# Optimization experiments

Measured on AMD Instinct MI355X. Metric: run time of the kernel, lower is better.

The kernel has to match this reference:

```python
import jax, jax.numpy as jnp
import numpy as np

N_NODES = 10000
N_EDGES = 70000
H = 128
L = 15  # message_passing_num
NODE_IN = 11  # 2 frame dims + 9 one-hot node types
EDGE_IN = 3
LN_EPS = 1e-5


def _mlp(x, W1, b1, W2, b2):
    return jax.nn.relu(x @ W1 + b1) @ W2 + b2


def _mlp_ln(x, W1, b1, W2, b2, g, b):
    h = _mlp(x, W1, b1, W2, b2)
    mu = jnp.mean(h, axis=-1, keepdims=True)
    var = jnp.var(h, axis=-1, keepdims=True)
    return (h - mu) * jax.lax.rsqrt(var + LN_EPS) * g + b


def setup_inputs() -> dict:
    key = jax.random.key(0)
    ks = iter(jax.random.split(key, 40))
    rn = lambda shp, s: (jax.random.normal(next(ks), shp, jnp.float32) * s)
    inp = {
        "node_type": jax.random.randint(next(ks), (N_NODES,), 0, 9, jnp.int32),
        "edge_index": jax.random.randint(next(ks), (2, N_EDGES), 0, N_NODES, jnp.int32),
        "frames": jax.random.normal(next(ks), (N_NODES, 2), jnp.float32),
        "edge_feats": jax.random.normal(next(ks), (N_EDGES, EDGE_IN), jnp.float32),
        "node_norm_mean": jax.random.normal(next(ks), (NODE_IN,), jnp.float32) * 0.1,
        "node_norm_std": jax.random.uniform(next(ks), (NODE_IN,), jnp.float32) + 0.5,
        "out_norm_mean": jax.random.normal(next(ks), (2,), jnp.float32) * 0.1,
        "out_norm_std": jax.random.uniform(next(ks), (2,), jnp.float32) + 0.5,
        # encoder node MLP (11 -> 128 -> 128, LayerNorm)
        "enc_nW1": rn((NODE_IN, H), NODE_IN ** -0.5), "enc_nb1": jnp.zeros((H,)),
        "enc_nW2": rn((H, H), H ** -0.5), "enc_nb2": jnp.zeros((H,)),
        "enc_nlng": jnp.ones((H,)), "enc_nlnb": jnp.zeros((H,)),
        # encoder edge MLP (3 -> 128 -> 128, LayerNorm)
        "enc_eW1": rn((EDGE_IN, H), EDGE_IN ** -0.5), "enc_eb1": jnp.zeros((H,)),
        "enc_eW2": rn((H, H), H ** -0.5), "enc_eb2": jnp.zeros((H,)),
        "enc_elng": jnp.ones((H,)), "enc_elnb": jnp.zeros((H,)),
        # L GNN blocks, stacked. Edge MLP: 3H -> H -> H (+LN); Node MLP: 2H -> H -> H (+LN)
        "eb_W1": rn((L, 3 * H, H), (3 * H) ** -0.5), "eb_b1": jnp.zeros((L, H)),
        "eb_W2": rn((L, H, H), H ** -0.5), "eb_b2": jnp.zeros((L, H)),
        "eb_lng": jnp.ones((L, H)), "eb_lnb": jnp.zeros((L, H)),
        "nb_W1": rn((L, 2 * H, H), (2 * H) ** -0.5), "nb_b1": jnp.zeros((L, H)),
        "nb_W2": rn((L, H, H), H ** -0.5), "nb_b2": jnp.zeros((L, H)),
        "nb_lng": jnp.ones((L, H)), "nb_lnb": jnp.zeros((L, H)),
        # decoder MLP (128 -> 128 -> 2, no LayerNorm)
        "dec_W1": rn((H, H), H ** -0.5), "dec_b1": jnp.zeros((H,)),
        "dec_W2": rn((H, 2), H ** -0.5), "dec_b2": jnp.zeros((2,)),
    }
    return inp


def reference(node_type, edge_index, frames, edge_feats,
              node_norm_mean, node_norm_std, out_norm_mean, out_norm_std,
              enc_nW1, enc_nb1, enc_nW2, enc_nb2, enc_nlng, enc_nlnb,
              enc_eW1, enc_eb1, enc_eW2, enc_eb2, enc_elng, enc_elnb,
              eb_W1, eb_b1, eb_W2, eb_b2, eb_lng, eb_lnb,
              nb_W1, nb_b1, nb_W2, nb_b2, nb_lng, nb_lnb,
              dec_W1, dec_b1, dec_W2, dec_b2):
    n_nodes = frames.shape[0]
    senders, receivers = edge_index[0], edge_index[1]

    # update_node_attr: concat(frames, one_hot(type, 9)) then normalize (eval mode)
    one_hot = jax.nn.one_hot(node_type, 9, dtype=frames.dtype)
    node_feats = jnp.concatenate([frames, one_hot], axis=1)  # [N, 11]
    node_attr = (node_feats - node_norm_mean) / node_norm_std

    # Encoder
    x = _mlp_ln(node_attr, enc_nW1, enc_nb1, enc_nW2, enc_nb2, enc_nlng, enc_nlnb)   # [N, H]
    e = _mlp_ln(edge_feats, enc_eW1, enc_eb1, enc_eW2, enc_eb2, enc_elng, enc_elnb)  # [E, H]

    # Processor: L residual GNN blocks (EdgeBlock then NodeBlock)
    def block(carry, p):
        x, e = carry
        (eW1, eb1, eW2, eb2, eg, ebn, nW1, nb1, nW2, nb2, ng, nbn) = p
        e_in = jnp.concatenate([x[senders], x[receivers], e], axis=-1)  # [E, 3H]
        e_new = _mlp_ln(e_in, eW1, eb1, eW2, eb2, eg, ebn)              # [E, H]
        agg = jax.ops.segment_sum(e_new, receivers, num_segments=n_nodes)  # [N, H]
        x_new = _mlp_ln(jnp.concatenate([x, agg], axis=-1), nW1, nb1, nW2, nb2, ng, nbn)
        return (x + x_new, e + e_new), None

    (x, e), _ = jax.lax.scan(
        block, (x, e),
        (eb_W1, eb_b1, eb_W2, eb_b2, eb_lng, eb_lnb,
         nb_W1, nb_b1, nb_W2, nb_b2, nb_lng, nb_lnb))

    # Decoder (no LayerNorm) + inverse output normalization (eval path)
    decoded = _mlp(x, dec_W1, dec_b1, dec_W2, dec_b2)  # [N, 2]
    velocity_update = decoded * out_norm_std + out_norm_mean
    return frames + velocity_update
```

## Files before the change

### kernel.cpp

```cpp
#include <hip/hip_runtime.h>
#include <hip/hip_bf16.h>

#define N_NODES 10000
#define N_EDGES 70000
#define NPAD 10112
#define EPAD 70016
#define H 128
#define NLAYERS 15
constexpr float LN_EPS = 1e-5f;

typedef __attribute__((ext_vector_type(8))) short short8;
typedef __attribute__((ext_vector_type(4))) float f32x4;

__device__ __forceinline__ float bf2f(unsigned int ulo16) {
    return __uint_as_float(ulo16 << 16);
}
__device__ __forceinline__ unsigned short f2bf(float f) {
    unsigned int x = __float_as_uint(f);
    x += 0x7fffu + ((x >> 16) & 1u);
    return (unsigned short)(x >> 16);
}

__global__ void prep_node(const int* __restrict__ nt, const float* __restrict__ frames,
                          const float* __restrict__ nm, const float* __restrict__ ns,
                          unsigned short* __restrict__ a16b) {
    int i = blockIdx.x * blockDim.x + threadIdx.x;
    if (i >= NPAD * 32) return;
    int n = i >> 5, k = i & 31;
    float v = 0.f;
    if (n < N_NODES && k < 11) {
        float raw = (k < 2) ? frames[n * 2 + k] : ((nt[n] == (k - 2)) ? 1.f : 0.f);
        v = (raw - nm[k]) / ns[k];
    }
    a16b[i] = f2bf(v);
}

__global__ void prep_edge(const float* __restrict__ ef, unsigned short* __restrict__ a4b) {
    int i = blockIdx.x * blockDim.x + threadIdx.x;
    if (i >= EPAD * 32) return;
    int e = i >> 5, k = i & 31;
    float v = (e < N_EDGES && k < 3) ? ef[e * 3 + k] : 0.f;
    a4b[i] = f2bf(v);
}

__global__ void transpose_w_tiled(const float* __restrict__ w, unsigned short* __restrict__ wt,
                                  int Kr, int Kp, int nmat) {
    __shared__ float T[32][33];
    int nkt = Kp / 32;
    int bid = blockIdx.x;
    int m = bid / (nkt * 4);
    int rest = bid % (nkt * 4);
    int kt = rest / 4, ct = rest % 4;
    int t = threadIdx.x;
    int tc = t & 31, tr = t >> 5;
#pragma unroll
    for (int rr = 0; rr < 4; ++rr) {
        int k = kt * 32 + tr + rr * 8;
        int c = ct * 32 + tc;
        T[tr + rr * 8][tc] = (k < Kr) ? w[((size_t)m * Kr + k) * H + c] : 0.f;
    }
    __syncthreads();
#pragma unroll
    for (int rr = 0; rr < 4; ++rr) {
        int c = ct * 32 + tr + rr * 8;
        int k = kt * 32 + tc;
        wt[((size_t)m * H + c) * Kp + k] = f2bf(T[tc][tr + rr * 8]);
    }
}

__global__ void hist_kernel(const int* __restrict__ rcv, int* __restrict__ counts) {
    int j = blockIdx.x * blockDim.x + threadIdx.x;
    if (j < N_EDGES) atomicAdd(&counts[rcv[j]], 1);
}

__global__ void scan_kernel(const int* __restrict__ counts, int* __restrict__ starts) {
    __shared__ int part[1024];
    const int CH = 10;
    int t = threadIdx.x;
    int base = t * CH;
    int loc[CH];
    int s = 0;
#pragma unroll
    for (int i = 0; i < CH; i++) {
        int idx = base + i;
        int c = (idx < N_NODES) ? counts[idx] : 0;
        loc[i] = s;
        s += c;
    }
    part[t] = s;
    __syncthreads();
    for (int off = 1; off < 1024; off <<= 1) {
        int v = (t >= off) ? part[t - off] : 0;
        __syncthreads();
        part[t] += v;
        __syncthreads();
    }
    int pre = (t > 0) ? part[t - 1] : 0;
#pragma unroll
    for (int i = 0; i < CH; i++) {
        int idx = base + i;
        if (idx < N_NODES) starts[idx] = pre + loc[i];
    }
}

__global__ void scatter_kernel(const int* __restrict__ rcv, const int* __restrict__ starts,
                               int* __restrict__ cursor, int* __restrict__ esorted) {
    int j = blockIdx.x * blockDim.x + threadIdx.x;
    if (j >= N_EDGES) return;
    int r = rcv[j];
    int p = starts[r] + atomicAdd(&cursor[r], 1);
    esorted[p] = j;
}

__global__ void agg_kernel(const unsigned short* __restrict__ enew,
                           const int* __restrict__ esorted,
                           const int* __restrict__ starts,
                           const int* __restrict__ counts,
                           unsigned short* __restrict__ aggb) {
    int n = blockIdx.x * 8 + (threadIdx.x >> 5);
    int l = threadIdx.x & 31;
    if (n >= N_NODES) return;
    float a0 = 0.f, a1 = 0.f, a2 = 0.f, a3 = 0.f;
    int s0 = starts[n], cnt = counts[n];
    for (int j = 0; j < cnt; ++j) {
        int e = esorted[s0 + j];
        uint2 v = *reinterpret_cast<const uint2*>(enew + (size_t)e * H + l * 4);
        a0 += bf2f(v.x & 0xffffu);
        a1 += bf2f(v.x >> 16);
        a2 += bf2f(v.y & 0xffffu);
        a3 += bf2f(v.y >> 16);
    }
    uint2 o;
    o.x = (unsigned int)f2bf(a0) | ((unsigned int)f2bf(a1) << 16);
    o.y = (unsigned int)f2bf(a2) | ((unsigned int)f2bf(a3) << 16);
    *reinterpret_cast<uint2*>(aggb + (size_t)n * H + l * 4) = o;
}

template <int K1, int AMODE, int EPI, int WR>
__launch_bounds__(256)
__global__ void mlp_fused(const unsigned short* __restrict__ A,
                          const unsigned short* __restrict__ Xb,
                          const unsigned short* __restrict__ Eb,
                          const unsigned short* __restrict__ Gb,
                          const int* __restrict__ snd,
                          const int* __restrict__ rcv,
                          const unsigned short* __restrict__ Bt1,
                          const float* __restrict__ bias1,
                          const unsigned short* __restrict__ Bt2,
                          const float* __restrict__ bias2,
                          const float* __restrict__ lng,
                          const float* __restrict__ lnb,
                          unsigned short* __restrict__ out_bf,
                          float* __restrict__ out_fp,
                          unsigned short* __restrict__ enew_bf,
                          int nrows) {
    constexpr int BK1 = (K1 >= 64) ? 64 : K1;
    constexpr int SA = BK1 + 8;
    constexpr int SB = 72;
    constexpr int SH = H + 8;
    constexpr int BM = 64 * WR;
    __shared__ __attribute__((aligned(16))) unsigned short As[BM * SA];
    __shared__ __attribute__((aligned(16))) unsigned short Bs[H * SB];
    __shared__ __attribute__((aligned(16))) unsigned short Hs[BM * SH];

    const int tid = threadIdx.x;
    const int wave = tid >> 6;
    const int lane = tid & 63;
    const int l15 = lane & 15;
    const int lhi = lane >> 4;
    const int row0 = blockIdx.x * BM;
    const int wrow = wave * 16 * WR;

    f32x4 acc[WR][8];
#pragma unroll
    for (int i = 0; i < WR; i++)
#pragma unroll
        for (int j = 0; j < 8; j++) acc[i][j] = (f32x4){0.f, 0.f, 0.f, 0.f};

    for (int kc = 0; kc < K1; kc += BK1) {
        constexpr int KQ = BK1 / 8;
        constexpr int LPT_A = BM * KQ / 256;
#pragma unroll
        for (int it = 0; it < LPT_A; ++it) {
            int q = tid + it * 256;
            int r = q / KQ;
            int kq = q % KQ;
            int gk = kc + kq * 8;
            int grow = row0 + r;
            const unsigned short* src;
            if (AMODE == 0) {
                src = A + (size_t)grow * K1 + gk;
            } else if (AMODE == 1) {
                int e = (grow < nrows) ? grow : 0;
                if (gk < H)          src = Xb + (size_t)snd[e] * H + gk;
                else if (gk < 2 * H) src = Xb + (size_t)rcv[e] * H + (gk - H);
                else                 src = Eb + (size_t)grow * H + (gk - 2 * H);
            } else {
                if (gk < H) src = Xb + (size_t)grow * H + gk;
                else        src = Gb + (size_t)grow * H + (gk - H);
            }
            uint4 v = *reinterpret_cast<const uint4*>(src);
            *reinterpret_cast<uint4*>(&As[r * SA + kq * 8]) = v;
        }
        constexpr int LPT_B = H * KQ / 256;
#pragma unroll
        for (int it = 0; it < LPT_B; ++it) {
            int q = tid + it * 256;
            int c = q / KQ;
            int kq = q % KQ;
            uint4 v = *reinterpret_cast<const uint4*>(Bt1 + (size_t)c * K1 + kc + kq * 8);
            *reinterpret_cast<uint4*>(&Bs[c * SB + kq * 8]) = v;
        }
        __syncthreads();
#pragma unroll
        for (int ks = 0; ks < BK1 / 32; ++ks) {
            short8 af[WR];
#pragma unroll
            for (int i = 0; i < WR; ++i)
                af[i] = *reinterpret_cast<const short8*>(
                    &As[(wrow + i * 16 + l15) * SA + ks * 32 + lhi * 8]);
#pragma unroll
            for (int j = 0; j < 8; ++j) {
                short8 bfr = *reinterpret_cast<const short8*>(
                    &Bs[(j * 16 + l15) * SB + ks * 32 + lhi * 8]);
#pragma unroll
                for (int i = 0; i < WR; ++i)
                    acc[i][j] = __builtin_amdgcn_mfma_f32_16x16x32_bf16(af[i], bfr, acc[i][j], 0, 0, 0);
            }
        }
        __syncthreads();
    }

    {
        float b1v[8];
#pragma unroll
        for (int j = 0; j < 8; ++j) b1v[j] = bias1[j * 16 + l15];
#pragma unroll
        for (int i = 0; i < WR; ++i)
#pragma unroll
            for (int r = 0; r < 4; ++r) {
                int rl = wrow + i * 16 + lhi * 4 + r;
#pragma unroll
                for (int j = 0; j < 8; ++j) {
                    float v = acc[i][j][r] + b1v[j];
                    Hs[rl * SH + j * 16 + l15] = f2bf(v > 0.f ? v : 0.f);
                }
            }
    }

#pragma unroll
    for (int i = 0; i < WR; i++)
#pragma unroll
        for (int j = 0; j < 8; j++) acc[i][j] = (f32x4){0.f, 0.f, 0.f, 0.f};

    for (int kc = 0; kc < H; kc += 64) {
        __syncthreads();
#pragma unroll
        for (int it = 0; it < 4; ++it) {
            int q = tid + it * 256;
            int c = q >> 3;
            int kq = q & 7;
            uint4 v = *reinterpret_cast<const uint4*>(Bt2 + (size_t)c * H + kc + kq * 8);
            *reinterpret_cast<uint4*>(&Bs[c * SB + kq * 8]) = v;
        }
        __syncthreads();
#pragma unroll
        for (int ks = 0; ks < 2; ++ks) {
            short8 af[WR];
#pragma unroll
            for (int i = 0; i < WR; ++i)
                af[i] = *reinterpret_cast<const short8*>(
                    &Hs[(wrow + i * 16 + l15) * SH + kc + ks * 32 + lhi * 8]);
#pragma unroll
            for (int j = 0; j < 8; ++j) {
                short8 bfr = *reinterpret_cast<const short8*>(
                    &Bs[(j * 16 + l15) * SB + ks * 32 + lhi * 8]);
#pragma unroll
                for (int i = 0; i < WR; ++i)
                    acc[i][j] = __builtin_amdgcn_mfma_f32_16x16x32_bf16(af[i], bfr, acc[i][j], 0, 0, 0);
            }
        }
    }

    float bv[8], gv[8], lv[8];
#pragma unroll
    for (int j = 0; j < 8; ++j) {
        bv[j] = bias2[j * 16 + l15];
        gv[j] = lng[j * 16 + l15];
        lv[j] = lnb[j * 16 + l15];
    }

#pragma unroll
    for (int i = 0; i < WR; ++i) {
#pragma unroll
        for (int r = 0; r < 4; ++r) {
            int row = row0 + wrow + i * 16 + lhi * 4 + r;
            float v[8];
            float s = 0.f, s2 = 0.f;
#pragma unroll
            for (int j = 0; j < 8; ++j) {
                v[j] = acc[i][j][r] + bv[j];
                s += v[j];
                s2 += v[j] * v[j];
            }
#pragma unroll
            for (int m = 1; m < 16; m <<= 1) {
                s += __shfl_xor(s, m);
                s2 += __shfl_xor(s2, m);
            }
            float mean = s * (1.f / 128.f);
            float var = s2 * (1.f / 128.f) - mean * mean;
            float rstd = rsqrtf(var + LN_EPS);
            if (row < nrows) {
#pragma unroll
                for (int j = 0; j < 8; ++j) {
                    float o = (v[j] - mean) * rstd * gv[j] + lv[j];
                    size_t off = (size_t)row * H + j * 16 + l15;
                    if (EPI == 1) {
                        out_fp[off] = o;
                        out_bf[off] = f2bf(o);
                    } else if (EPI == 2) {
                        float nx = out_fp[off] + o;
                        out_fp[off] = nx;
                        out_bf[off] = f2bf(nx);
                    } else {
                        float ne = out_fp[off] + o;
                        out_fp[off] = ne;
                        out_bf[off] = f2bf(ne);
                        enew_bf[off] = f2bf(o);
                    }
                }
            }
        }
    }
}

__global__ void decoder_kernel(const float* __restrict__ x,
                               const float* __restrict__ frames,
                               const float* __restrict__ W1, const float* __restrict__ b1,
                               const float* __restrict__ W2, const float* __restrict__ b2,
                               const float* __restrict__ omean, const float* __restrict__ ostd,
                               float* __restrict__ outp) {
    __shared__ float xr[H];
    __shared__ float hr[H];
    __shared__ float red[2][2];
    int n = blockIdx.x;
    int t = threadIdx.x;
    xr[t] = x[n * H + t];
    __syncthreads();
    float acc = 0.f;
#pragma unroll 8
    for (int k = 0; k < H; k++) acc += xr[k] * W1[k * H + t];
    hr[t] = fmaxf(acc + b1[t], 0.f);
    __syncthreads();
    float p0 = hr[t] * W2[t * 2 + 0];
    float p1 = hr[t] * W2[t * 2 + 1];
#pragma unroll
    for (int m = 1; m < 64; m <<= 1) {
        p0 += __shfl_xor(p0, m);
        p1 += __shfl_xor(p1, m);
    }
    if ((t & 63) == 0) { red[t >> 6][0] = p0; red[t >> 6][1] = p1; }
    __syncthreads();
    if (t < 2) {
        float d = red[0][t] + red[1][t] + b2[t];
        outp[n * 2 + t] = frames[n * 2 + t] + d * ostd[t] + omean[t];
    }
}

extern "C" void kernel_launch(void* const* d_in, const int* in_sizes, int n_in,
                              void* d_out, int out_size, void* d_ws, size_t ws_size,
                              hipStream_t stream) {
    (void)in_sizes; (void)n_in; (void)out_size; (void)ws_size;
    const int*   node_type  = (const int*)  d_in[0];
    const int*   edge_index = (const int*)  d_in[1];
    const float* frames     = (const float*)d_in[2];
    const float* edge_feats = (const float*)d_in[3];
    const float* nmean      = (const float*)d_in[4];
    const float* nstd       = (const float*)d_in[5];
    const float* omean      = (const float*)d_in[6];
    const float* ostd       = (const float*)d_in[7];
    const float* enc_nW1    = (const float*)d_in[8];
    const float* enc_nb1    = (const float*)d_in[9];
    const float* enc_nW2    = (const float*)d_in[10];
    const float* enc_nb2    = (const float*)d_in[11];
    const float* enc_nlng   = (const float*)d_in[12];
    const float* enc_nlnb   = (const float*)d_in[13];
    const float* enc_eW1    = (const float*)d_in[14];
    const float* enc_eb1    = (const float*)d_in[15];
    const float* enc_eW2    = (const float*)d_in[16];
    const float* enc_eb2    = (const float*)d_in[17];
    const float* enc_elng   = (const float*)d_in[18];
    const float* enc_elnb   = (const float*)d_in[19];
    const float* eb_W1      = (const float*)d_in[20];
    const float* eb_b1      = (const float*)d_in[21];
    const float* eb_W2      = (const float*)d_in[22];
    const float* eb_b2      = (const float*)d_in[23];
    const float* eb_g       = (const float*)d_in[24];
    const float* eb_bn      = (const float*)d_in[25];
    const float* nb_W1      = (const float*)d_in[26];
    const float* nb_b1      = (const float*)d_in[27];
    const float* nb_W2      = (const float*)d_in[28];
    const float* nb_b2      = (const float*)d_in[29];
    const float* nb_g       = (const float*)d_in[30];
    const float* nb_bn      = (const float*)d_in[31];
    const float* dec_W1     = (const float*)d_in[32];
    const float* dec_b1     = (const float*)d_in[33];
    const float* dec_W2     = (const float*)d_in[34];
    const float* dec_b2     = (const float*)d_in[35];

    const int* snd = edge_index;
    const int* rcv = edge_index + N_EDGES;

    char* p = (char*)d_ws;
    auto alloc = [&](size_t bytes) {
        void* r = (void*)p;
        p += (bytes + 255) & ~(size_t)255;
        return r;
    };
    float* x_fp  = (float*)alloc((size_t)NPAD * H * 4);
    float* e_fp  = (float*)alloc((size_t)EPAD * H * 4);
    unsigned short* x_bf   = (unsigned short*)alloc((size_t)NPAD * H * 2);
    unsigned short* e_bf   = (unsigned short*)alloc((size_t)EPAD * H * 2);
    unsigned short* enew   = (unsigned short*)alloc((size_t)EPAD * H * 2);
    unsigned short* agg_bf = (unsigned short*)alloc((size_t)NPAD * H * 2);
    unsigned short* a16b   = (unsigned short*)alloc((size_t)NPAD * 32 * 2);
    unsigned short* a4b    = (unsigned short*)alloc((size_t)EPAD * 32 * 2);
    unsigned short* wt_en1 = (unsigned short*)alloc((size_t)128 * 32 * 2);
    unsigned short* wt_ee1 = (unsigned short*)alloc((size_t)128 * 32 * 2);
    unsigned short* wt_en2 = (unsigned short*)alloc((size_t)128 * 128 * 2);
    unsigned short* wt_ee2 = (unsigned short*)alloc((size_t)128 * 128 * 2);
    unsigned short* wt_eb1 = (unsigned short*)alloc((size_t)NLAYERS * 128 * 384 * 2);
    unsigned short* wt_eb2 = (unsigned short*)alloc((size_t)NLAYERS * 128 * 128 * 2);
    unsigned short* wt_nb1 = (unsigned short*)alloc((size_t)NLAYERS * 128 * 256 * 2);
    unsigned short* wt_nb2 = (unsigned short*)alloc((size_t)NLAYERS * 128 * 128 * 2);
    int* counts  = (int*)alloc((size_t)N_NODES * 4);
    int* starts  = (int*)alloc((size_t)N_NODES * 4);
    int* cursor  = (int*)alloc((size_t)N_NODES * 4);
    int* esorted = (int*)alloc((size_t)N_EDGES * 4);

    prep_node<<<(NPAD * 32 + 255) / 256, 256, 0, stream>>>(node_type, frames, nmean, nstd, a16b);
    prep_edge<<<(EPAD * 32 + 255) / 256, 256, 0, stream>>>(edge_feats, a4b);
    auto tw = [&](const float* w, unsigned short* wt, int Kr, int Kp, int nmat) {
        int blocks = nmat * (Kp / 32) * 4;
        transpose_w_tiled<<<blocks, 256, 0, stream>>>(w, wt, Kr, Kp, nmat);
    };
    tw(enc_nW1, wt_en1, 11, 32, 1);
    tw(enc_eW1, wt_ee1, 3, 32, 1);
    tw(enc_nW2, wt_en2, 128, 128, 1);
    tw(enc_eW2, wt_ee2, 128, 128, 1);
    tw(eb_W1, wt_eb1, 384, 384, NLAYERS);
    tw(eb_W2, wt_eb2, 128, 128, NLAYERS);
    tw(nb_W1, wt_nb1, 256, 256, NLAYERS);
    tw(nb_W2, wt_nb2, 128, 128, NLAYERS);

    hipMemsetAsync(counts, 0, (size_t)N_NODES * 4, stream);
    hipMemsetAsync(cursor, 0, (size_t)N_NODES * 4, stream);
    hist_kernel<<<(N_EDGES + 255) / 256, 256, 0, stream>>>(rcv, counts);
    scan_kernel<<<1, 1024, 0, stream>>>(counts, starts);
    scatter_kernel<<<(N_EDGES + 255) / 256, 256, 0, stream>>>(rcv, starts, cursor, esorted);

    const int gE = EPAD / 128;
    const int gN = NPAD / 64;
    const unsigned short* nu_ = nullptr;
    const int* ni_ = nullptr;
    unsigned short* nm_ = nullptr;

    mlp_fused<32, 0, 1, 1><<<gN, 256, 0, stream>>>(a16b, nu_, nu_, nu_, ni_, ni_,
        wt_en1, enc_nb1, wt_en2, enc_nb2, enc_nlng, enc_nlnb,
        x_bf, x_fp, nm_, N_NODES);
    mlp_fused<32, 0, 1, 2><<<gE, 256, 0, stream>>>(a4b, nu_, nu_, nu_, ni_, ni_,
        wt_ee1, enc_eb1, wt_ee2, enc_eb2, enc_elng, enc_elnb,
        e_bf, e_fp, nm_, N_EDGES);

    for (int l = 0; l < NLAYERS; ++l) {
        mlp_fused<384, 1, 3, 2><<<gE, 256, 0, stream>>>(nu_, x_bf, e_bf, nu_, snd, rcv,
            wt_eb1 + (size_t)l * 128 * 384, eb_b1 + l * H,
            wt_eb2 + (size_t)l * 128 * 128, eb_b2 + l * H, eb_g + l * H, eb_bn + l * H,
            e_bf, e_fp, enew, N_EDGES);
        agg_kernel<<<(N_NODES + 7) / 8, 256, 0, stream>>>(enew, esorted, starts, counts, agg_bf);
        mlp_fused<256, 2, 2, 1><<<gN, 256, 0, stream>>>(nu_, x_bf, nu_, agg_bf, ni_, ni_,
            wt_nb1 + (size_t)l * 128 * 256, nb_b1 + l * H,
            wt_nb2 + (size_t)l * 128 * 128, nb_b2 + l * H, nb_g + l * H, nb_bn + l * H,
            x_bf, x_fp, nm_, N_NODES);
    }

    decoder_kernel<<<N_NODES, 128, 0, stream>>>(x_fp, frames, dec_W1, dec_b1, dec_W2, dec_b2,
                                                omean, ostd, (float*)d_out);
}
```

Baseline: 1.181 ms.

## Pre-swizzle weights into MFMA fragment layout and drop LDS staging in MLP kernel

Measured after the change: 1.418 ms. +20.1%, slower.

```diff
diff --git a/kernel.cpp b/kernel.cpp
--- a/kernel.cpp
+++ b/kernel.cpp
@@ -43,8 +43,8 @@
     a4b[i] = f2bf(v);
 }
 
-__global__ void transpose_w_tiled(const float* __restrict__ w, unsigned short* __restrict__ wt,
-                                  int Kr, int Kp, int nmat) {
+__global__ void transpose_w_frag(const float* __restrict__ w, unsigned short* __restrict__ wt,
+                                 int Kr, int Kp, int nmat) {
     __shared__ float T[32][33];
     int nkt = Kp / 32;
     int bid = blockIdx.x;
@@ -64,7 +64,9 @@
     for (int rr = 0; rr < 4; ++rr) {
         int c = ct * 32 + tr + rr * 8;
         int k = kt * 32 + tc;
-        wt[((size_t)m * H + c) * Kp + k] = f2bf(T[tc][tr + rr * 8]);
+        size_t fidx = ((((size_t)m * nkt + (k >> 5)) * 8 + (c >> 4)) * 64
+                       + ((k >> 3) & 3) * 16 + (c & 15)) * 8 + (k & 7);
+        wt[fidx] = f2bf(T[tc][tr + rr * 8]);
     }
 }
 
@@ -117,118 +119,104 @@
                            const int* __restrict__ starts,
                            const int* __restrict__ counts,
                            unsigned short* __restrict__ aggb) {
-    int n = blockIdx.x * 8 + (threadIdx.x >> 5);
-    int l = threadIdx.x & 31;
+    int n = blockIdx.x * 16 + (threadIdx.x >> 4);
+    int l = threadIdx.x & 15;
     if (n >= N_NODES) return;
-    float a0 = 0.f, a1 = 0.f, a2 = 0.f, a3 = 0.f;
+    float a[8];
+#pragma unroll
+    for (int q = 0; q < 8; ++q) a[q] = 0.f;
     int s0 = starts[n], cnt = counts[n];
     for (int j = 0; j < cnt; ++j) {
         int e = esorted[s0 + j];
-        uint2 v = *reinterpret_cast<const uint2*>(enew + (size_t)e * H + l * 4);
-        a0 += bf2f(v.x & 0xffffu);
-        a1 += bf2f(v.x >> 16);
-        a2 += bf2f(v.y & 0xffffu);
-        a3 += bf2f(v.y >> 16);
-    }
-    uint2 o;
-    o.x = (unsigned int)f2bf(a0) | ((unsigned int)f2bf(a1) << 16);
-    o.y = (unsigned int)f2bf(a2) | ((unsigned int)f2bf(a3) << 16);
-    *reinterpret_cast<uint2*>(aggb + (size_t)n * H + l * 4) = o;
-}
-
-template <int K1, int AMODE, int EPI, int WR>
+        uint4 v = *reinterpret_cast<const uint4*>(enew + (size_t)e * H + l * 8);
+        a[0] += bf2f(v.x & 0xffffu); a[1] += bf2f(v.x >> 16);
+        a[2] += bf2f(v.y & 0xffffu); a[3] += bf2f(v.y >> 16);
+        a[4] += bf2f(v.z & 0xffffu); a[5] += bf2f(v.z >> 16);
+        a[6] += bf2f(v.w & 0xffffu); a[7] += bf2f(v.w >> 16);
+    }
+    uint4 o;
+    o.x = (unsigned int)f2bf(a[0]) | ((unsigned int)f2bf(a[1]) << 16);
+    o.y = (unsigned int)f2bf(a[2]) | ((unsigned int)f2bf(a[3]) << 16);
+    o.z = (unsigned int)f2bf(a[4]) | ((unsigned int)f2bf(a[5]) << 16);
+    o.w = (unsigned int)f2bf(a[6]) | ((unsigned int)f2bf(a[7]) << 16);
+    *reinterpret_cast<uint4*>(aggb + (size_t)n * H + l * 8) = o;
+}
+
+template <int K1, int AMODE, int EPI, int RW>
 __launch_bounds__(256)
-__global__ void mlp_fused(const unsigned short* __restrict__ A,
-                          const unsigned short* __restrict__ Xb,
-                          const unsigned short* __restrict__ Eb,
-                          const unsigned short* __restrict__ Gb,
-                          const int* __restrict__ snd,
-                          const int* __restrict__ rcv,
-                          const unsigned short* __restrict__ Bt1,
-                          const float* __restrict__ bias1,
-                          const unsigned short* __restrict__ Bt2,
-                          const float* __restrict__ bias2,
-                          const float* __restrict__ lng,
-                          const float* __restrict__ lnb,
-                          unsigned short* __restrict__ out_bf,
-                          float* __restrict__ out_fp,
-                          unsigned short* __restrict__ enew_bf,
-                          int nrows) {
-    constexpr int BK1 = (K1 >= 64) ? 64 : K1;
-    constexpr int SA = BK1 + 8;
-    constexpr int SB = 72;
+__global__ void mlp_wave(const unsigned short* __restrict__ A,
+                         const unsigned short* __restrict__ Xb,
+                         const unsigned short* __restrict__ Eb,
+                         const unsigned short* __restrict__ Gb,
+                         const int* __restrict__ snd,
+                         const int* __restrict__ rcv,
+                         const unsigned short* __restrict__ Bt1,
+                         const float* __restrict__ bias1,
+                         const unsigned short* __restrict__ Bt2,
+                         const float* __restrict__ bias2,
+                         const float* __restrict__ lng,
+                         const float* __restrict__ lnb,
+                         unsigned short* __restrict__ out_bf,
+                         float* __restrict__ out_fp,
+                         unsigned short* __restrict__ enew_bf,
+                         int nrows) {
     constexpr int SH = H + 8;
-    constexpr int BM = 64 * WR;
-    __shared__ __attribute__((aligned(16))) unsigned short As[BM * SA];
-    __shared__ __attribute__((aligned(16))) unsigned short Bs[H * SB];
-    __shared__ __attribute__((aligned(16))) unsigned short Hs[BM * SH];
+    __shared__ __attribute__((aligned(16))) unsigned short Hs[4 * 16 * RW * SH];
 
     const int tid = threadIdx.x;
     const int wave = tid >> 6;
     const int lane = tid & 63;
     const int l15 = lane & 15;
     const int lhi = lane >> 4;
-    const int row0 = blockIdx.x * BM;
-    const int wrow = wave * 16 * WR;
-
-    f32x4 acc[WR][8];
-#pragma unroll
-    for (int i = 0; i < WR; i++)
+    const int wrow0 = (blockIdx.x * 4 + wave) * (16 * RW);
+    unsigned short* Hw = Hs + wave * (16 * RW) * SH;
+
+    const unsigned short* pS[RW];
+    const unsigned short* pR[RW];
+    const unsigned short* pE[RW];
+#pragma unroll
+    for (int i = 0; i < RW; ++i) {
+        int grow = wrow0 + i * 16 + l15;
+        if (AMODE == 0) {
+            pS[i] = A + (size_t)grow * K1;
+        } else if (AMODE == 1) {
+            int e = (grow < nrows) ? grow : (nrows - 1);
+            pS[i] = Xb + (size_t)snd[e] * H;
+            pR[i] = Xb + (size_t)rcv[e] * H;
+            pE[i] = Eb + (size_t)grow * H;
+        } else {
+            pS[i] = Xb + (size_t)grow * H;
+            pR[i] = Gb + (size_t)grow * H;
+        }
+    }
+
+    f32x4 acc[RW][8];
+#pragma unroll
+    for (int i = 0; i < RW; i++)
 #pragma unroll
         for (int j = 0; j < 8; j++) acc[i][j] = (f32x4){0.f, 0.f, 0.f, 0.f};
 
-    for (int kc = 0; kc < K1; kc += BK1) {
-        constexpr int KQ = BK1 / 8;
-        constexpr int LPT_A = BM * KQ / 256;
-#pragma unroll
-        for (int it = 0; it < LPT_A; ++it) {
-            int q = tid + it * 256;
-            int r = q / KQ;
-            int kq = q % KQ;
-            int gk = kc + kq * 8;
-            int grow = row0 + r;
-            const unsigned short* src;
-            if (AMODE == 0) {
-                src = A + (size_t)grow * K1 + gk;
-            } else if (AMODE == 1) {
-                int e = (grow < nrows) ? grow : 0;
-                if (gk < H)          src = Xb + (size_t)snd[e] * H + gk;
-                else if (gk < 2 * H) src = Xb + (size_t)rcv[e] * H + (gk - H);
-                else                 src = Eb + (size_t)grow * H + (gk - 2 * H);
-            } else {
-                if (gk < H) src = Xb + (size_t)grow * H + gk;
-                else        src = Gb + (size_t)grow * H + (gk - H);
-            }
-            uint4 v = *reinterpret_cast<const uint4*>(src);
-            *reinterpret_cast<uint4*>(&As[r * SA + kq * 8]) = v;
+#pragma unroll 4
+    for (int kc = 0; kc < K1; kc += 32) {
+        short8 af[RW];
+#pragma unroll
+        for (int i = 0; i < RW; ++i) {
+            const unsigned short* s;
+            if (AMODE == 0)      s = pS[i] + kc;
+            else if (AMODE == 1) s = (kc < H) ? pS[i] + kc
+                                 : (kc < 2 * H) ? pR[i] + (kc - H)
+                                 : pE[i] + (kc - 2 * H);
+            else                 s = (kc < H) ? pS[i] + kc : pR[i] + (kc - H);
+            af[i] = *reinterpret_cast<const short8*>(s + lhi * 8);
         }
-        constexpr int LPT_B = H * KQ / 256;
-#pragma unroll
-        for (int it = 0; it < LPT_B; ++it) {
-            int q = tid + it * 256;
-            int c = q / KQ;
-            int kq = q % KQ;
-            uint4 v = *reinterpret_cast<const uint4*>(Bt1 + (size_t)c * K1 + kc + kq * 8);
-            *reinterpret_cast<uint4*>(&Bs[c * SB + kq * 8]) = v;
+        const unsigned short* bbase = Bt1 + ((size_t)(kc >> 5) * 8) * 512 + lane * 8;
+#pragma unroll
+        for (int j = 0; j < 8; ++j) {
+            short8 bfr = *reinterpret_cast<const short8*>(bbase + j * 512);
+#pragma unroll
+            for (int i = 0; i < RW; ++i)
+                acc[i][j] = __builtin_amdgcn_mfma_f32_16x16x32_bf16(af[i], bfr, acc[i][j], 0, 0, 0);
         }
-        __syncthreads();
-#pragma unroll
-        for (int ks = 0; ks < BK1 / 32; ++ks) {
-            short8 af[WR];
-#pragma unroll
-            for (int i = 0; i < WR; ++i)
-                af[i] = *reinterpret_cast<const short8*>(
-                    &As[(wrow + i * 16 + l15) * SA + ks * 32 + lhi * 8]);
-#pragma unroll
-            for (int j = 0; j < 8; ++j) {
-                short8 bfr = *reinterpret_cast<const short8*>(
-                    &Bs[(j * 16 + l15) * SB + ks * 32 + lhi * 8]);
-#pragma unroll
-                for (int i = 0; i < WR; ++i)
-                    acc[i][j] = __builtin_amdgcn_mfma_f32_16x16x32_bf16(af[i], bfr, acc[i][j], 0, 0, 0);
-            }
-        }
-        __syncthreads();
     }
 
     {
@@ -236,49 +224,36 @@
 #pragma unroll
         for (int j = 0; j < 8; ++j) b1v[j] = bias1[j * 16 + l15];
 #pragma unroll
-        for (int i = 0; i < WR; ++i)
+        for (int i = 0; i < RW; ++i)
 #pragma unroll
             for (int r = 0; r < 4; ++r) {
-                int rl = wrow + i * 16 + lhi * 4 + r;
+                int rl = i * 16 + lhi * 4 + r;
 #pragma unroll
                 for (int j = 0; j < 8; ++j) {
                     float v = acc[i][j][r] + b1v[j];
-                    Hs[rl * SH + j * 16 + l15] = f2bf(v > 0.f ? v : 0.f);
+                    Hw[rl * SH + j * 16 + l15] = f2bf(v > 0.f ? v : 0.f);
                 }
             }
     }
 
 #pragma unroll
-    for (int i = 0; i < WR; i++)
+    for (int i = 0; i < RW; i++)
 #pragma unroll
         for (int j = 0; j < 8; j++) acc[i][j] = (f32x4){0.f, 0.f, 0.f, 0.f};
 
-    for (int kc = 0; kc < H; kc += 64) {
-        __syncthreads();
-#pragma unroll
-        for (int it = 0; it < 4; ++it) {
-            int q = tid + it * 256;
-            int c = q >> 3;
-            int kq = q & 7;
-            uint4 v = *reinterpret_cast<const uint4*>(Bt2 + (size_t)c * H + kc + kq * 8);
-            *reinterpret_cast<uint4*>(&Bs[c * SB + kq * 8]) = v;
-        }
-        __syncthreads();
-#pragma unroll
-        for (int ks = 0; ks < 2; ++ks) {
-            short8 af[WR];
-#pragma unroll
-            for (int i = 0; i < WR; ++i)
-                af[i] = *reinterpret_cast<const short8*>(
-                    &Hs[(wrow + i * 16 + l15) * SH + kc + ks * 32 + lhi * 8]);
-#pragma unroll
-            for (int j = 0; j < 8; ++j) {
-                short8 bfr = *reinterpret_cast<const short8*>(
-                    &Bs[(j * 16 + l15) * SB + ks * 32 + lhi * 8]);
-#pragma unroll
-                for (int i = 0; i < WR; ++i)
-                    acc[i][j] = __builtin_amdgcn_mfma_f32_16x16x32_bf16(af[i], bfr, acc[i][j], 0, 0, 0);
-            }
+#pragma unroll
+    for (int kc = 0; kc < H; kc += 32) {
+        short8 af[RW];
+#pragma unroll
+        for (int i = 0; i < RW; ++i)
+            af[i] = *reinterpret_cast<const short8*>(&Hw[(i * 16 + l15) * SH + kc + lhi * 8]);
+        const unsigned short* bbase = Bt2 + ((size_t)(kc >> 5) * 8) * 512 + lane * 8;
+#pragma unroll
+        for (int j = 0; j < 8; ++j) {
+            short8 bfr = *reinterpret_cast<const short8*>(bbase + j * 512);
+#pragma unroll
+            for (int i = 0; i < RW; ++i)
+                acc[i][j] = __builtin_amdgcn_mfma_f32_16x16x32_bf16(af[i], bfr, acc[i][j], 0, 0, 0);
         }
     }
 
@@ -291,10 +266,10 @@
     }
 
 #pragma unroll
-    for (int i = 0; i < WR; ++i) {
+    for (int i = 0; i < RW; ++i) {
 #pragma unroll
         for (int r = 0; r < 4; ++r) {
-            int row = row0 + wrow + i * 16 + lhi * 4 + r;
+            int row = wrow0 + i * 16 + lhi * 4 + r;
             float v[8];
             float s = 0.f, s2 = 0.f;
 #pragma unroll
@@ -443,7 +418,7 @@
     prep_edge<<<(EPAD * 32 + 255) / 256, 256, 0, stream>>>(edge_feats, a4b);
     auto tw = [&](const float* w, unsigned short* wt, int Kr, int Kp, int nmat) {
         int blocks = nmat * (Kp / 32) * 4;
-        transpose_w_tiled<<<blocks, 256, 0, stream>>>(w, wt, Kr, Kp, nmat);
+        transpose_w_frag<<<blocks, 256, 0, stream>>>(w, wt, Kr, Kp, nmat);
     };
     tw(enc_nW1, wt_en1, 11, 32, 1);
     tw(enc_eW1, wt_ee1, 3, 32, 1);
@@ -466,20 +441,20 @@
     const int* ni_ = nullptr;
     unsigned short* nm_ = nullptr;
 
-    mlp_fused<32, 0, 1, 1><<<gN, 256, 0, stream>>>(a16b, nu_, nu_, nu_, ni_, ni_,
+    mlp_wave<32, 0, 1, 1><<<gN, 256, 0, stream>>>(a16b, nu_, nu_, nu_, ni_, ni_,
         wt_en1, enc_nb1, wt_en2, enc_nb2, enc_nlng, enc_nlnb,
         x_bf, x_fp, nm_, N_NODES);
-    mlp_fused<32, 0, 1, 2><<<gE, 256, 0, stream>>>(a4b, nu_, nu_, nu_, ni_, ni_,
+    mlp_wave<32, 0, 1, 2><<<gE, 256, 0, stream>>>(a4b, nu_, nu_, nu_, ni_, ni_,
         wt_ee1, enc_eb1, wt_ee2, enc_eb2, enc_elng, enc_elnb,
         e_bf, e_fp, nm_, N_EDGES);
 
     for (int l = 0; l < NLAYERS; ++l) {
-        mlp_fused<384, 1, 3, 2><<<gE, 256, 0, stream>>>(nu_, x_bf, e_bf, nu_, snd, rcv,
+        mlp_wave<384, 1, 3, 2><<<gE, 256, 0, stream>>>(nu_, x_bf, e_bf, nu_, snd, rcv,
             wt_eb1 + (size_t)l * 128 * 384, eb_b1 + l * H,
             wt_eb2 + (size_t)l * 128 * 128, eb_b2 + l * H, eb_g + l * H, eb_bn + l * H,
             e_bf, e_fp, enew, N_EDGES);
-        agg_kernel<<<(N_NODES + 7) / 8, 256, 0, stream>>>(enew, esorted, starts, counts, agg_bf);
-        mlp_fused<256, 2, 2, 1><<<gN, 256, 0, stream>>>(nu_, x_bf, nu_, agg_bf, ni_, ni_,
+        agg_kernel<<<(N_NODES + 15) / 16, 256, 0, stream>>>(enew, esorted, starts, counts, agg_bf);
+        mlp_wave<256, 2, 2, 1><<<gN, 256, 0, stream>>>(nu_, x_bf, nu_, agg_bf, ni_, ni_,
             wt_nb1 + (size_t)l * 128 * 256, nb_b1 + l * H,
             wt_nb2 + (size_t)l * 128 * 128, nb_b2 + l * H, nb_g + l * H, nb_bn + l * H,
             x_bf, x_fp, nm_, N_NODES);
```
